# Kernel optimization log

Hardware: AMD Instinct MI355X
Metric: run time of the kernel (lower is better)

Reference implementation:

```python
import jax, jax.numpy as jnp
import numpy as np

N_NODES = 50000
IN_DIM = 128
OUT_DIM = 128
HEADS = 4
HEAD_DIM = OUT_DIM // HEADS
N_EDGES = 800000
LN_EPS = 1e-5
NEG_SLOPE = 0.2


def setup_inputs() -> dict:
    key = jax.random.key(0)
    ks = jax.random.split(key, 8)
    x = jax.random.normal(ks[0], (N_NODES, IN_DIM), dtype=jnp.float32)
    edge_index = jax.random.randint(ks[1], (2, N_EDGES), 0, N_NODES, dtype=jnp.int64)
    s = 1.0 / np.sqrt(IN_DIM)
    W = jax.random.uniform(ks[2], (IN_DIM, HEADS * HEAD_DIM), jnp.float32, -s, s)
    att_src = jax.random.uniform(ks[3], (HEADS, HEAD_DIM), jnp.float32, -s, s)
    att_dst = jax.random.uniform(ks[4], (HEADS, HEAD_DIM), jnp.float32, -s, s)
    bias = jnp.zeros((OUT_DIM,), jnp.float32)
    gamma = jnp.ones((OUT_DIM,), jnp.float32)
    beta = jnp.zeros((OUT_DIM,), jnp.float32)
    return {"x": x, "edge_index": edge_index, "W": W, "att_src": att_src,
            "att_dst": att_dst, "bias": bias, "gamma": gamma, "beta": beta}


def reference(x, edge_index, W, att_src, att_dst, bias, gamma, beta):
    N = x.shape[0]
    H, C = att_src.shape
    # add self-loops (PyG GATConv default)
    loops = jnp.arange(N, dtype=edge_index.dtype)
    src = jnp.concatenate([edge_index[0], loops])  # [E+N]
    dst = jnp.concatenate([edge_index[1], loops])

    h = (x @ W).reshape(N, H, C)                      # [N,H,C]
    a_src = jnp.einsum('nhc,hc->nh', h, att_src)      # [N,H]
    a_dst = jnp.einsum('nhc,hc->nh', h, att_dst)

    e = jax.nn.leaky_relu(a_src[src] + a_dst[dst], NEG_SLOPE)   # [E+N,H]
    emax = jax.ops.segment_max(e, dst, num_segments=N)          # [N,H]
    ex = jnp.exp(e - emax[dst])
    denom = jax.ops.segment_sum(ex, dst, num_segments=N)
    alpha = ex / denom[dst]                                     # [E+N,H]

    msg = h[src] * alpha[:, :, None]                            # [E+N,H,C]
    out = jax.ops.segment_sum(msg, dst, num_segments=N).reshape(N, H * C) + bias

    # LayerNorm
    mu = out.mean(-1, keepdims=True)
    var = ((out - mu) ** 2).mean(-1, keepdims=True)
    hn = (out - mu) / jnp.sqrt(var + LN_EPS) * gamma + beta

    # residual is Identity (in_dim == out_dim); GELU exact; dropout = eval identity
    return jax.nn.gelu(hn + x, approximate=False)
```

## Files before the change

### kernel.cpp

```cpp
#include <hip/hip_runtime.h>
#include <math.h>

#define N_NODES 50000
#define HEADS 4
#define NEG_SLOPE 0.2f
#define LN_EPS 1e-5f
#define SLOTS 80
#define GR 64
#define EPB 2048

typedef short short8 __attribute__((ext_vector_type(8)));
typedef float f32x4 __attribute__((ext_vector_type(4)));


__device__ __forceinline__ short f2bf(float f) {
    unsigned u = __float_as_uint(f);
    return (short)((u + 0x7fffu + ((u >> 16) & 1u)) >> 16);
}

__device__ __forceinline__ void load_edge(const int* __restrict__ ei, int e, int E,
                                          int is64, int& s, int& d) {
    if (is64) {
        s = ei[2 * e];
        d = ei[2 * (E + e)];
    } else {
        s = ei[e];
        d = ei[E + e];
    }
}

__device__ __forceinline__ int detect_is64(const int* __restrict__ ei, int t, int* s_flag) {
    if (t < 64) {
        int nz = (ei[2 * t + 1] != 0) ? 1 : 0;
        unsigned long long b = __ballot(nz);
        if (t == 0) *s_flag = (b == 0ULL) ? 1 : 0;
    }
    __syncthreads();
    return *s_flag;
}

__device__ __forceinline__ float s8f(unsigned u, int p) {
    return (float)((int)(u << (24 - 8 * p)) >> 24);
}

__device__ __forceinline__ float edge_w(float v) {
    v = v > 0.f ? v : NEG_SLOPE * v;
    return __expf(v);
}

__device__ __forceinline__ void scatter_one(const int* __restrict__ ei, int e, int E,
                                            int is64, int* __restrict__ cnt,
                                            unsigned short* __restrict__ esrc) {
    if (e >= E) return;
    int s, d;
    load_edge(ei, e, E, is64, s, d);
    int p = atomicAdd(&cnt[d], 1);
    if (p < SLOTS) esrc[d * SLOTS + p] = (unsigned short)s;
}


__global__ __launch_bounds__(256, 4) void gemm_scatter_kernel(
    const float* __restrict__ x, const float* __restrict__ W,
    const float* __restrict__ att_src, const float* __restrict__ att_dst,
    unsigned* __restrict__ hb, float* __restrict__ hscale,
    float* __restrict__ a_src, float* __restrict__ a_dst,
    const int* __restrict__ ei, int E, int nScatter, int nGemm,
    int* __restrict__ cnt, unsigned short* __restrict__ esrc) {
    __shared__ __align__(16) char smem[40960];
    const int t = threadIdx.x;
    const int b = (int)blockIdx.x;

    const bool isScatter = (b % 3) == 0;
    const int rid = isScatter ? (b / 3) : (2 * (b / 3) + (b % 3) - 1);

    if (isScatter) {
        if (rid >= nScatter) return;
        int is64 = detect_is64(ei, t, (int*)smem);
        const int e0 = rid * EPB + t;
#pragma unroll
        for (int u = 0; u < 8; ++u)
            scatter_one(ei, e0 + u * 256, E, is64, cnt, esrc);
        return;
    }

    if (rid >= nGemm) return;
    const int rowBase = rid * GR;
    const int l = t & 63;
    const int wv = t >> 6;

    {
        const int nlo = l & 7, khi = l >> 3;
        for (int i = 0; i < 8; ++i) {
            int tile = wv + 4 * i;
            int n = (tile & 15) * 8 + nlo;
            int k8 = (tile >> 4) * 8 + khi;
            short8 pk;
#pragma unroll
            for (int jj = 0; jj < 8; ++jj)
                pk[jj] = f2bf(W[(k8 * 8 + jj) * 128 + n]);
            int us = (k8 & 8) | ((k8 & 7) ^ (n & 7));
            *(short8*)(smem + n * 256 + us * 16) = pk;
        }
    }
    __syncthreads();

    const int g = l >> 4;
    const int c = l & 15;

    f32x4 acc[8];
#pragma unroll
    for (int ct = 0; ct < 8; ++ct) acc[ct] = {0.f, 0.f, 0.f, 0.f};

    {
        int arow = rowBase + wv * 16 + c;
        if (arow >= N_NODES) arow = N_NODES - 1;
        const float* xrow = x + (size_t)arow * 128;
#pragma unroll
        for (int kk = 0; kk < 4; ++kk) {
            float4 xa = *(const float4*)(xrow + kk * 32 + g * 8);
            float4 xb = *(const float4*)(xrow + kk * 32 + g * 8 + 4);
            short8 af;
            af[0] = f2bf(xa.x); af[1] = f2bf(xa.y); af[2] = f2bf(xa.z); af[3] = f2bf(xa.w);
            af[4] = f2bf(xb.x); af[5] = f2bf(xb.y); af[6] = f2bf(xb.z); af[7] = f2bf(xb.w);
#pragma unroll
            for (int ct = 0; ct < 8; ++ct) {
                int n = ct * 16 + c;
                int u = kk * 4 + g;
                int us = (u & 8) | ((u & 7) ^ (n & 7));
                short8 bf = *(const short8*)(smem + n * 256 + us * 16);
                acc[ct] = __builtin_amdgcn_mfma_f32_16x16x32_bf16(af, bf, acc[ct], 0, 0, 0);
            }
        }
    }

    char* ep = smem + 32768 + wv * 2048;
    float asA[4], asB[4], adA[4], adB[4];
#pragma unroll
    for (int h = 0; h < 4; ++h) {
        asA[h] = att_src[h * 32 + c];
        asB[h] = att_src[h * 32 + 16 + c];
        adA[h] = att_dst[h * 32 + c];
        adB[h] = att_dst[h * 32 + 16 + c];
    }
#pragma unroll
    for (int r = 0; r < 4; ++r) {
        float v[8];
#pragma unroll
        for (int ct = 0; ct < 8; ++ct) v[ct] = acc[ct][r];

        float m = fabsf(v[0]);
#pragma unroll
        for (int ct = 1; ct < 8; ++ct) m = fmaxf(m, fabsf(v[ct]));
#pragma unroll
        for (int o = 1; o < 16; o <<= 1) m = fmaxf(m, __shfl_xor(m, o, 64));
        m = fmaxf(m, 1e-20f);
        const float inv = 127.0f / m;

        float sp[4], dp[4];
#pragma unroll
        for (int h = 0; h < 4; ++h) {
            sp[h] = v[2 * h] * asA[h] + v[2 * h + 1] * asB[h];
            dp[h] = v[2 * h] * adA[h] + v[2 * h + 1] * adB[h];
        }
#pragma unroll
        for (int o = 1; o < 16; o <<= 1) {
#pragma unroll
            for (int h = 0; h < 4; ++h) {
                sp[h] += __shfl_xor(sp[h], o, 64);
                dp[h] += __shfl_xor(dp[h], o, 64);
            }
        }
        const int row_l = g * 4 + r;
        const int row = rowBase + wv * 16 + row_l;
        if (c == 0 && row < N_NODES) {
            hscale[row] = m * (1.0f / 127.0f);
            a_src[row * 4 + 0] = sp[0]; a_src[row * 4 + 1] = sp[1];
            a_src[row * 4 + 2] = sp[2]; a_src[row * 4 + 3] = sp[3];
            a_dst[row * 4 + 0] = dp[0]; a_dst[row * 4 + 1] = dp[1];
            a_dst[row * 4 + 2] = dp[2]; a_dst[row * 4 + 3] = dp[3];
        }
#pragma unroll
        for (int ct = 0; ct < 8; ++ct) {
            int q = __float2int_rn(v[ct] * inv);
            ep[row_l * 128 + ct * 16 + c] = (char)q;
        }
    }

#pragma unroll
    for (int w8 = 0; w8 < 8; ++w8) {
        int idx = w8 * 64 + l;
        int row_l = idx >> 5, tx = idx & 31;
        unsigned word = *(const unsigned*)(ep + row_l * 128 + tx * 4);
        int row = rowBase + wv * 16 + row_l;
        if (row < N_NODES) hb[(size_t)row * 32 + tx] = word;
    }
}

__global__ __launch_bounds__(256) void gat_fused_kernel(
    const int* __restrict__ cnt, const unsigned short* __restrict__ esrc,
    const float* __restrict__ a_src, const float* __restrict__ a_dst,
    const unsigned* __restrict__ hb, const float* __restrict__ hscale,
    const float* __restrict__ bias, const float* __restrict__ x,
    const float* __restrict__ gamma, const float* __restrict__ beta,
    float* __restrict__ out) {
    const int t = threadIdx.x;
    const int l = t & 63;
    const int wv = t >> 6;
    const int g = l >> 4;
    const int j = l & 15;
    const int n = blockIdx.x * 16 + wv * 4 + g;
    const int hh = j >> 2;

    const uint2* hb2 = (const uint2*)hb;

    const float adst_me = a_dst[(n << 2) + hh];
    float ps = edge_w(a_src[(n << 2) + hh] + adst_me);

    uint2 hvS = hb2[(unsigned)(n * 16 + j)];
    {
        const float uS = ps * hscale[n];
        float acc0 = uS * s8f(hvS.x, 0), acc1 = uS * s8f(hvS.x, 1);
        float acc2 = uS * s8f(hvS.x, 2), acc3 = uS * s8f(hvS.x, 3);
        float acc4 = uS * s8f(hvS.y, 0), acc5 = uS * s8f(hvS.y, 1);
        float acc6 = uS * s8f(hvS.y, 2), acc7 = uS * s8f(hvS.y, 3);

        const int deg = min(cnt[n], SLOTS);
        const unsigned short* row = esrc + n * SLOTS;

        for (int base = 0; base < deg; base += 8) {
            const int rem = deg - base;
            uint4 q = *(const uint4*)(row + base);
            int s0 = (int)(q.x & 0xffffu);
            int s1 = (rem > 1) ? (int)(q.x >> 16) : n;
            int s2 = (rem > 2) ? (int)(q.y & 0xffffu) : n;
            int s3 = (rem > 3) ? (int)(q.y >> 16) : n;
            int s4 = (rem > 4) ? (int)(q.z & 0xffffu) : n;
            int s5 = (rem > 5) ? (int)(q.z >> 16) : n;
            int s6 = (rem > 6) ? (int)(q.w & 0xffffu) : n;
            int s7 = (rem > 7) ? (int)(q.w >> 16) : n;

            float b0 = a_src[(s0 << 2) + hh];
            float b1 = a_src[(s1 << 2) + hh];
            float b2 = a_src[(s2 << 2) + hh];
            float b3 = a_src[(s3 << 2) + hh];
            float b4 = a_src[(s4 << 2) + hh];
            float b5 = a_src[(s5 << 2) + hh];
            float b6 = a_src[(s6 << 2) + hh];
            float b7 = a_src[(s7 << 2) + hh];
            float c0 = hscale[s0], c1 = hscale[s1], c2 = hscale[s2], c3 = hscale[s3];
            float c4 = hscale[s4], c5 = hscale[s5], c6 = hscale[s6], c7 = hscale[s7];
            uint2 h0 = hb2[(unsigned)(s0 * 16 + j)];
            uint2 h1 = hb2[(unsigned)(s1 * 16 + j)];
            uint2 h2 = hb2[(unsigned)(s2 * 16 + j)];
            uint2 h3 = hb2[(unsigned)(s3 * 16 + j)];
            uint2 h4 = hb2[(unsigned)(s4 * 16 + j)];
            uint2 h5 = hb2[(unsigned)(s5 * 16 + j)];
            uint2 h6 = hb2[(unsigned)(s6 * 16 + j)];
            uint2 h7 = hb2[(unsigned)(s7 * 16 + j)];

            float w0 = edge_w(b0 + adst_me);
            float w1 = (rem > 1) ? edge_w(b1 + adst_me) : 0.f;
            float w2 = (rem > 2) ? edge_w(b2 + adst_me) : 0.f;
            float w3 = (rem > 3) ? edge_w(b3 + adst_me) : 0.f;
            float w4 = (rem > 4) ? edge_w(b4 + adst_me) : 0.f;
            float w5 = (rem > 5) ? edge_w(b5 + adst_me) : 0.f;
            float w6 = (rem > 6) ? edge_w(b6 + adst_me) : 0.f;
            float w7 = (rem > 7) ? edge_w(b7 + adst_me) : 0.f;
            ps += (w0 + w1 + w2 + w3) + (w4 + w5 + w6 + w7);

            float u0 = w0 * c0, u1 = w1 * c1, u2 = w2 * c2, u3 = w3 * c3;
            float u4 = w4 * c4, u5 = w5 * c5, u6 = w6 * c6, u7 = w7 * c7;

            acc0 += u0 * s8f(h0.x, 0) + u1 * s8f(h1.x, 0) + u2 * s8f(h2.x, 0) + u3 * s8f(h3.x, 0)
                  + u4 * s8f(h4.x, 0) + u5 * s8f(h5.x, 0) + u6 * s8f(h6.x, 0) + u7 * s8f(h7.x, 0);
            acc1 += u0 * s8f(h0.x, 1) + u1 * s8f(h1.x, 1) + u2 * s8f(h2.x, 1) + u3 * s8f(h3.x, 1)
                  + u4 * s8f(h4.x, 1) + u5 * s8f(h5.x, 1) + u6 * s8f(h6.x, 1) + u7 * s8f(h7.x, 1);
            acc2 += u0 * s8f(h0.x, 2) + u1 * s8f(h1.x, 2) + u2 * s8f(h2.x, 2) + u3 * s8f(h3.x, 2)
                  + u4 * s8f(h4.x, 2) + u5 * s8f(h5.x, 2) + u6 * s8f(h6.x, 2) + u7 * s8f(h7.x, 2);
            acc3 += u0 * s8f(h0.x, 3) + u1 * s8f(h1.x, 3) + u2 * s8f(h2.x, 3) + u3 * s8f(h3.x, 3)
                  + u4 * s8f(h4.x, 3) + u5 * s8f(h5.x, 3) + u6 * s8f(h6.x, 3) + u7 * s8f(h7.x, 3);
            acc4 += u0 * s8f(h0.y, 0) + u1 * s8f(h1.y, 0) + u2 * s8f(h2.y, 0) + u3 * s8f(h3.y, 0)
                  + u4 * s8f(h4.y, 0) + u5 * s8f(h5.y, 0) + u6 * s8f(h6.y, 0) + u7 * s8f(h7.y, 0);
            acc5 += u0 * s8f(h0.y, 1) + u1 * s8f(h1.y, 1) + u2 * s8f(h2.y, 1) + u3 * s8f(h3.y, 1)
                  + u4 * s8f(h4.y, 1) + u5 * s8f(h5.y, 1) + u6 * s8f(h6.y, 1) + u7 * s8f(h7.y, 1);
            acc6 += u0 * s8f(h0.y, 2) + u1 * s8f(h1.y, 2) + u2 * s8f(h2.y, 2) + u3 * s8f(h3.y, 2)
                  + u4 * s8f(h4.y, 2) + u5 * s8f(h5.y, 2) + u6 * s8f(h6.y, 2) + u7 * s8f(h7.y, 2);
            acc7 += u0 * s8f(h0.y, 3) + u1 * s8f(h1.y, 3) + u2 * s8f(h2.y, 3) + u3 * s8f(h3.y, 3)
                  + u4 * s8f(h4.y, 3) + u5 * s8f(h5.y, 3) + u6 * s8f(h6.y, 3) + u7 * s8f(h7.y, 3);
        }

        const float inv = 1.0f / ps;
        const float4* bias4 = (const float4*)bias;
        float4 bA = bias4[j * 2], bB = bias4[j * 2 + 1];
        float v0 = acc0 * inv + bA.x, v1 = acc1 * inv + bA.y;
        float v2 = acc2 * inv + bA.z, v3 = acc3 * inv + bA.w;
        float v4 = acc4 * inv + bB.x, v5 = acc5 * inv + bB.y;
        float v6 = acc6 * inv + bB.z, v7 = acc7 * inv + bB.w;

        float s1 = v0 + v1 + v2 + v3 + v4 + v5 + v6 + v7;
        float s2 = v0 * v0 + v1 * v1 + v2 * v2 + v3 * v3 +
                   v4 * v4 + v5 * v5 + v6 * v6 + v7 * v7;
#pragma unroll
        for (int o = 1; o < 16; o <<= 1) {
            s1 += __shfl_xor(s1, o, 64);
            s2 += __shfl_xor(s2, o, 64);
        }
        float mu = s1 * (1.0f / 128.0f);
        float var = s2 * (1.0f / 128.0f) - mu * mu;
        float rstd = rsqrtf(var + LN_EPS);

        const float4* gamma4 = (const float4*)gamma;
        const float4* beta4 = (const float4*)beta;
        const float4* x4 = (const float4*)x;
        float4 gA = gamma4[j * 2], gB = gamma4[j * 2 + 1];
        float4 eA = beta4[j * 2], eB = beta4[j * 2 + 1];
        float4 xA = x4[(size_t)n * 32 + j * 2], xB = x4[(size_t)n * 32 + j * 2 + 1];

        float r0 = (v0 - mu) * rstd * gA.x + eA.x + xA.x;
        float r1 = (v1 - mu) * rstd * gA.y + eA.y + xA.y;
        float r2 = (v2 - mu) * rstd * gA.z + eA.z + xA.z;
        float r3 = (v3 - mu) * rstd * gA.w + eA.w + xA.w;
        float r4 = (v4 - mu) * rstd * gB.x + eB.x + xB.x;
        float r5 = (v5 - mu) * rstd * gB.y + eB.y + xB.y;
        float r6 = (v6 - mu) * rstd * gB.z + eB.z + xB.z;
        float r7 = (v7 - mu) * rstd * gB.w + eB.w + xB.w;

        const float k = 0.70710678118654752440f;
        float4 oA = make_float4(0.5f * r0 * (1.0f + erff(r0 * k)),
                                0.5f * r1 * (1.0f + erff(r1 * k)),
                                0.5f * r2 * (1.0f + erff(r2 * k)),
                                0.5f * r3 * (1.0f + erff(r3 * k)));
        float4 oB = make_float4(0.5f * r4 * (1.0f + erff(r4 * k)),
                                0.5f * r5 * (1.0f + erff(r5 * k)),
                                0.5f * r6 * (1.0f + erff(r6 * k)),
                                0.5f * r7 * (1.0f + erff(r7 * k)));
        float4* out4 = (float4*)out;
        out4[(size_t)n * 32 + j * 2] = oA;
        out4[(size_t)n * 32 + j * 2 + 1] = oB;
    }
}


extern "C" void kernel_launch(void* const* d_in, const int* in_sizes, int n_in,
                              void* d_out, int out_size, void* d_ws, size_t ws_size,
                              hipStream_t stream) {
    const float* x       = (const float*)d_in[0];
    const int*   ei      = (const int*)d_in[1];
    const float* W       = (const float*)d_in[2];
    const float* att_src = (const float*)d_in[3];
    const float* att_dst = (const float*)d_in[4];
    const float* bias    = (const float*)d_in[5];
    const float* gamma   = (const float*)d_in[6];
    const float* beta    = (const float*)d_in[7];
    float* out = (float*)d_out;
    const int E = in_sizes[1] / 2;

    unsigned* hb         = (unsigned*)d_ws;
    float* hscale        = (float*)(hb + (size_t)N_NODES * 32);
    float* a_src         = hscale + N_NODES;
    float* a_dst         = a_src + N_NODES * 4;
    int*   cnt           = (int*)(a_dst + N_NODES * 4);
    unsigned short* esrc = (unsigned short*)(cnt + N_NODES);

    const int nScatter = (E + EPB - 1) / EPB;
    const int nGemm = (N_NODES + GR - 1) / GR;
    int total = 3 * nScatter;
    const int needGemm = 3 * ((nGemm + 1) / 2);
    if (needGemm > total) total = needGemm;

    hipMemsetAsync(cnt, 0, N_NODES * sizeof(int), stream);
    gemm_scatter_kernel<<<total, 256, 0, stream>>>(
        x, W, att_src, att_dst, hb, hscale, a_src, a_dst, ei, E, nScatter, nGemm,
        cnt, esrc);
    gat_fused_kernel<<<N_NODES / 16, 256, 0, stream>>>(cnt, esrc, a_src, a_dst, hb,
                                                       hscale, bias, x, gamma, beta, out);
}
```

Measured before the change: 167.0 us.

## Replace global-atomic edge scatter with two-pass LDS bucket binning and build kernel

Edges are first binned per block into 256-node destination buckets with shared-memory atomics and written to a staging buffer. A new build kernel then processes one bucket per block, using LDS atomics to fill the per-destination source lists and write counts. This replaces per-edge global atomics and the counter memset. In exchange it adds an extra kernel launch and a staging round trip. A per-cell cap can silently drop edges if a block's bucket overflows.

```diff
diff --git a/kernel.cpp b/kernel.cpp
--- a/kernel.cpp
+++ b/kernel.cpp
@@ -8,6 +8,9 @@
 #define SLOTS 80
 #define GR 64
 #define EPB 2048
+#define DSH 8
+#define NB 196
+#define CAP 40
 
 typedef short short8 __attribute__((ext_vector_type(8)));
 typedef float f32x4 __attribute__((ext_vector_type(4)));
@@ -48,16 +51,6 @@
     return __expf(v);
 }
 
-__device__ __forceinline__ void scatter_one(const int* __restrict__ ei, int e, int E,
-                                            int is64, int* __restrict__ cnt,
-                                            unsigned short* __restrict__ esrc) {
-    if (e >= E) return;
-    int s, d;
-    load_edge(ei, e, E, is64, s, d);
-    int p = atomicAdd(&cnt[d], 1);
-    if (p < SLOTS) esrc[d * SLOTS + p] = (unsigned short)s;
-}
-
 
 __global__ __launch_bounds__(256, 4) void gemm_scatter_kernel(
     const float* __restrict__ x, const float* __restrict__ W,
@@ -65,21 +58,44 @@
     unsigned* __restrict__ hb, float* __restrict__ hscale,
     float* __restrict__ a_src, float* __restrict__ a_dst,
     const int* __restrict__ ei, int E, int nScatter, int nGemm,
-    int* __restrict__ cnt, unsigned short* __restrict__ esrc) {
+    unsigned* __restrict__ staging, int* __restrict__ scnt) {
     __shared__ __align__(16) char smem[40960];
     const int t = threadIdx.x;
     const int b = (int)blockIdx.x;
 
-    const bool isScatter = (b % 3) == 0;
-    const int rid = isScatter ? (b / 3) : (2 * (b / 3) + (b % 3) - 1);
-
-    if (isScatter) {
+    const bool isBin = (b % 3) == 0;
+    const int rid = isBin ? (b / 3) : (2 * (b / 3) + (b % 3) - 1);
+
+    if (isBin) {
         if (rid >= nScatter) return;
         int is64 = detect_is64(ei, t, (int*)smem);
+        int* lcnt = (int*)smem + 64;
+        for (int i = t; i < NB; i += 256) lcnt[i] = 0;
+        __syncthreads();
+
         const int e0 = rid * EPB + t;
-#pragma unroll
-        for (int u = 0; u < 8; ++u)
-            scatter_one(ei, e0 + u * 256, E, is64, cnt, esrc);
+        int ss[8], dd[8];
+#pragma unroll
+        for (int u = 0; u < 8; ++u) {
+            int e = e0 + u * 256;
+            if (e < E) {
+                load_edge(ei, e, E, is64, ss[u], dd[u]);
+            } else {
+                ss[u] = -1; dd[u] = 0;
+            }
+        }
+#pragma unroll
+        for (int u = 0; u < 8; ++u) {
+            if (ss[u] < 0) continue;
+            int bkt = dd[u] >> DSH;
+            int p = atomicAdd(&lcnt[bkt], 1);
+            if (p < CAP)
+                staging[((size_t)bkt * nScatter + rid) * CAP + p] =
+                    (unsigned)ss[u] | ((unsigned)dd[u] << 16);
+        }
+        __syncthreads();
+        for (int i = t; i < NB; i += 256)
+            scnt[(size_t)i * nScatter + rid] = min(lcnt[i], CAP);
         return;
     }
 
@@ -194,6 +210,48 @@
         int row = rowBase + wv * 16 + row_l;
         if (row < N_NODES) hb[(size_t)row * 32 + tx] = word;
     }
+}
+
+__global__ __launch_bounds__(256) void build_kernel(
+    const unsigned* __restrict__ staging, const int* __restrict__ scnt,
+    int nScatter, int* __restrict__ cnt, unsigned short* __restrict__ esrc) {
+    __shared__ int lcnt2[256];
+    const int B = blockIdx.x;
+    const int t = threadIdx.x;
+    lcnt2[t] = 0;
+    __syncthreads();
+
+    for (int blk = t; blk < nScatter; blk += 256) {
+        const int c = scnt[(size_t)B * nScatter + blk];
+        const unsigned* cell = staging + ((size_t)B * nScatter + blk) * CAP;
+        for (int j = 0; j < c; j += 4) {
+            uint4 q = *(const uint4*)(cell + j);
+            const int m = c - j;
+            {
+                int d = (int)(q.x >> 16);
+                int p = atomicAdd(&lcnt2[d & 255], 1);
+                if (p < SLOTS) esrc[(size_t)d * SLOTS + p] = (unsigned short)(q.x & 0xffffu);
+            }
+            if (m > 1) {
+                int d = (int)(q.y >> 16);
+                int p = atomicAdd(&lcnt2[d & 255], 1);
+                if (p < SLOTS) esrc[(size_t)d * SLOTS + p] = (unsigned short)(q.y & 0xffffu);
+            }
+            if (m > 2) {
+                int d = (int)(q.z >> 16);
+                int p = atomicAdd(&lcnt2[d & 255], 1);
+                if (p < SLOTS) esrc[(size_t)d * SLOTS + p] = (unsigned short)(q.z & 0xffffu);
+            }
+            if (m > 3) {
+                int d = (int)(q.w >> 16);
+                int p = atomicAdd(&lcnt2[d & 255], 1);
+                if (p < SLOTS) esrc[(size_t)d * SLOTS + p] = (unsigned short)(q.w & 0xffffu);
+            }
+        }
+    }
+    __syncthreads();
+    const int d = (B << DSH) + t;
+    if (d < N_NODES) cnt[d] = lcnt2[t];
 }
 
 __global__ __launch_bounds__(256) void gat_fused_kernel(
@@ -363,15 +421,18 @@
     unsigned short* esrc = (unsigned short*)(cnt + N_NODES);
 
     const int nScatter = (E + EPB - 1) / EPB;
+    unsigned* staging    = (unsigned*)(esrc + (size_t)N_NODES * SLOTS);
+    int* scnt            = (int*)(staging + (size_t)NB * nScatter * CAP);
+
     const int nGemm = (N_NODES + GR - 1) / GR;
     int total = 3 * nScatter;
     const int needGemm = 3 * ((nGemm + 1) / 2);
     if (needGemm > total) total = needGemm;
 
-    hipMemsetAsync(cnt, 0, N_NODES * sizeof(int), stream);
     gemm_scatter_kernel<<<total, 256, 0, stream>>>(
         x, W, att_src, att_dst, hb, hscale, a_src, a_dst, ei, E, nScatter, nGemm,
-        cnt, esrc);
+        staging, scnt);
+    build_kernel<<<NB, 256, 0, stream>>>(staging, scnt, nScatter, cnt, esrc);
     gat_fused_kernel<<<N_NODES / 16, 256, 0, stream>>>(cnt, esrc, a_src, a_dst, hb,
                                                        hscale, bias, x, gamma, beta, out);
 }
```

After: 147.3 us. 11.8% less time.
